# Kernel optimization log

Hardware: AMD Instinct MI355X
Metric: run time of the kernel (lower is better)

The kernel has to match this reference:

```python
import jax, jax.numpy as jnp
import numpy as np

BIG = 1e10  # penalty for cross-batch pairs in masked knn


def knn_interpolate(x, pos, pos_skip, batch, batch_skip, k):
    # squared pairwise distances [N_skip, N] via ||a||^2 + ||b||^2 - 2 a.b (avoids [Ns,N,3] temp)
    d2 = (jnp.sum(pos_skip**2, -1)[:, None]
          + jnp.sum(pos**2, -1)[None, :]
          - 2.0 * (pos_skip @ pos.T))
    d2 = jnp.maximum(d2, 0.0)
    # mask out neighbors from a different cloud in the batch
    d2 = d2 + jnp.where(batch_skip[:, None] != batch[None, :], BIG, 0.0)
    neg_d2k, idx = jax.lax.top_k(-d2, k)          # k smallest distances
    d2k = -neg_d2k                                # [N_skip, k]
    w = 1.0 / jnp.clip(d2k, 1e-16)                # inverse squared-distance weights (PyG convention)
    xk = x[idx]                                   # gather neighbor features [N_skip, k, C]
    return jnp.sum(w[..., None] * xk, axis=1) / jnp.sum(w, axis=1, keepdims=True)


def setup_inputs() -> dict:
    key = jax.random.key(0)
    ks = jax.random.split(key, 8)
    B, N, Ns, C, Cs, H = 4, 4096, 16384, 256, 128, 512
    x = jax.random.normal(ks[0], (N, C), dtype=jnp.float32)
    pos = jax.random.normal(ks[1], (N, 3), dtype=jnp.float32)
    batch = jnp.repeat(jnp.arange(B, dtype=jnp.int64), N // B)
    x_skip = jax.random.normal(ks[2], (Ns, Cs), dtype=jnp.float32)
    pos_skip = jax.random.normal(ks[3], (Ns, 3), dtype=jnp.float32)
    batch_skip = jnp.repeat(jnp.arange(B, dtype=jnp.int64), Ns // B)
    fan_in1, fan_in2 = C + Cs, H
    W1 = jax.random.normal(ks[4], (fan_in1, H), dtype=jnp.float32) / np.sqrt(fan_in1)
    b1 = jnp.zeros((H,), dtype=jnp.float32)
    W2 = jax.random.normal(ks[5], (H, H), dtype=jnp.float32) / np.sqrt(fan_in2)
    b2 = jnp.zeros((H,), dtype=jnp.float32)
    return {"x": x, "pos": pos, "batch": batch, "x_skip": x_skip,
            "pos_skip": pos_skip, "batch_skip": batch_skip,
            "W1": W1, "b1": b1, "W2": W2, "b2": b2, "k": 3}


def reference(x, pos, batch, x_skip, pos_skip, batch_skip, W1, b1, W2, b2, k):
    xi = knn_interpolate(x, pos, pos_skip, batch, batch_skip, k)  # [Ns, C]
    h = jnp.concatenate([xi, x_skip], axis=1)                     # [Ns, C+Cs]
    h = jax.nn.relu(h @ W1 + b1)
    h = jax.nn.relu(h @ W2 + b2)
    return (h, pos_skip, batch_skip)
```

## Files before the change

kernel.cpp:

```cpp
#include <hip/hip_runtime.h>
#include <hip/hip_bf16.h>
#include <float.h>


#define KNN_K 3
#define NBATCH 4

typedef __attribute__((ext_vector_type(8))) __bf16 bf16x8;
typedef __attribute__((ext_vector_type(4))) __bf16 bf16x4;
typedef __attribute__((ext_vector_type(4))) float  f32x4;
typedef unsigned long long ull;

__device__ __forceinline__ void gload_lds16(const void* g, void* l) {
    __builtin_amdgcn_global_load_lds(
        (const __attribute__((address_space(1))) unsigned int*)g,
        (__attribute__((address_space(3))) unsigned int*)l, 16, 0, 0);
}

template<int K>
__device__ __forceinline__ void insK(ull (&key)[K], ull c) {
    if (c < key[K-1]) {
        key[K-1] = c;
#pragma unroll
        for (int p = K-1; p >= 1; --p) {
            if (key[p] < key[p-1]) {
                ull t = key[p-1]; key[p-1] = key[p]; key[p] = t;
            }
        }
    }
}

template<int SPAN, int C, int Cs>
__global__ __launch_bounds__(256) void knn_wprep_fast(
    const float* __restrict__ x, const float* __restrict__ pos,
    const int* __restrict__ batch, const float* __restrict__ x_skip,
    const float* __restrict__ pos_skip, const int* __restrict__ batch_skip,
    __bf16* __restrict__ h0, float* __restrict__ out_tail, int Ns,
    const float* __restrict__ W1, const float* __restrict__ W2,
    __bf16* __restrict__ W1t, __bf16* __restrict__ W2t,
    int K1, int H, int H2, int knnBlocks)
{
    __shared__ float4 pos4[SPAN];
    __shared__ ull    skey[256 * KNN_K];
    __shared__ int    sidx[16][KNN_K];
    __shared__ float  swt [16][KNN_K + 1];
    __shared__ float  Ws[32][33];

    const int t = threadIdx.x;

    if (blockIdx.x >= knnBlocks) {
        int b = blockIdx.x - knnBlocks;
        const float* W; __bf16* Wt; int kt, nt, K, Ncols;
        const int nt1 = H / 32, n1 = (K1 / 32) * nt1;
        if (b < n1) { W = W1; Wt = W1t; K = K1; Ncols = H;  kt = b / nt1; nt = b % nt1; }
        else { b -= n1; const int nt2 = H2 / 32;
               W = W2; Wt = W2t; K = H;  Ncols = H2; kt = b / nt2; nt = b % nt2; }
        const int r = t >> 5, c = t & 31;
#pragma unroll
        for (int i = 0; i < 4; ++i)
            Ws[r + i*8][c] = W[(size_t)(kt*32 + r + i*8) * Ncols + nt*32 + c];
        __syncthreads();
#pragma unroll
        for (int i = 0; i < 4; ++i)
            Wt[(size_t)(nt*32 + r + i*8) * K + kt*32 + c] = (__bf16)Ws[c][r + i*8];
        return;
    }

    const int q0 = blockIdx.x * 16;
    const int bs    = batch_skip[q0];
    const int cbase = bs * SPAN;

    for (int i = t; i < SPAN; i += 256) {
        const int j = cbase + i;
        const float qx = pos[j*3+0], qy = pos[j*3+1], qz = pos[j*3+2];
        float pn2 = qx*qx + qy*qy + qz*qz;
        if (batch[j] != bs) pn2 = 3.0e38f;
        pos4[i] = make_float4(qx, qy, qz, pn2);
    }

    if (t < 48)               out_tail[q0*3 + t] = pos_skip[q0*3 + t];
    else if (t < 64)          out_tail[(size_t)Ns*3 + q0 + (t-48)] =
                                  (float)batch_skip[q0 + (t-48)];
    __syncthreads();

    const int q   = t & 15;
    const int g   = t >> 4;
    const int qq  = q0 + q;
    const float px = pos_skip[qq*3+0], py = pos_skip[qq*3+1], pz = pos_skip[qq*3+2];
    const float ps2 = px*px + py*py + pz*pz;

    ull kA[KNN_K], kB[KNN_K], kC[KNN_K], kD[KNN_K];
#pragma unroll
    for (int j = 0; j < KNN_K; ++j) { kA[j]=~0ull; kB[j]=~0ull; kC[j]=~0ull; kD[j]=~0ull; }

    const int base = g * (SPAN / 16);
#pragma unroll 4
    for (int i = 0; i < 16; ++i) {
        const int ii = (i + g) & 15;
        const int jA = base + ii;
        const int jB = base + 16 + ii;
        const int jC = base + 32 + ii;
        const int jD = base + 48 + ii;
        const float4 pA = pos4[jA];
        const float4 pB = pos4[jB];
        const float4 pC = pos4[jC];
        const float4 pD = pos4[jD];
        float d2A = (ps2 + pA.w) - 2.0f*(px*pA.x + py*pA.y + pz*pA.z);
        float d2B = (ps2 + pB.w) - 2.0f*(px*pB.x + py*pB.y + pz*pB.z);
        float d2C = (ps2 + pC.w) - 2.0f*(px*pC.x + py*pC.y + pz*pC.z);
        float d2D = (ps2 + pD.w) - 2.0f*(px*pD.x + py*pD.y + pz*pD.z);
        d2A = fmaxf(d2A, 0.0f); d2B = fmaxf(d2B, 0.0f);
        d2C = fmaxf(d2C, 0.0f); d2D = fmaxf(d2D, 0.0f);
        insK<KNN_K>(kA, ((ull)__float_as_uint(d2A) << 32) | (unsigned)(cbase + jA));
        insK<KNN_K>(kB, ((ull)__float_as_uint(d2B) << 32) | (unsigned)(cbase + jB));
        insK<KNN_K>(kC, ((ull)__float_as_uint(d2C) << 32) | (unsigned)(cbase + jC));
        insK<KNN_K>(kD, ((ull)__float_as_uint(d2D) << 32) | (unsigned)(cbase + jD));
    }
#pragma unroll
    for (int j = 0; j < KNN_K; ++j) insK<KNN_K>(kA, kB[j]);
#pragma unroll
    for (int j = 0; j < KNN_K; ++j) insK<KNN_K>(kA, kC[j]);
#pragma unroll
    for (int j = 0; j < KNN_K; ++j) insK<KNN_K>(kA, kD[j]);

#pragma unroll
    for (int j = 0; j < KNN_K; ++j) skey[t*KNN_K + j] = kA[j];
    __syncthreads();

    if (t < 16) {
        ull key[KNN_K];
#pragma unroll
        for (int j = 0; j < KNN_K; ++j) key[j] = skey[t*KNN_K + j];
#pragma unroll
        for (int gg = 1; gg < 16; ++gg)
#pragma unroll
            for (int j = 0; j < KNN_K; ++j)
                insK<KNN_K>(key, skey[(t + 16*gg)*KNN_K + j]);
        float wv[KNN_K]; float wsum = 0.0f;
#pragma unroll
        for (int j = 0; j < KNN_K; ++j) {
            const float d2 = __uint_as_float((unsigned)(key[j] >> 32));
            sidx[t][j] = (int)(key[j] & 0xFFFFFFFFull);
            wv[j] = 1.0f / fmaxf(d2, 1e-16f);
            wsum += wv[j];
            swt[t][j] = wv[j];
        }
        swt[t][KNN_K] = 1.0f / wsum;
    }
    __syncthreads();

    {
        const int gq  = t >> 4;
        const int sub = t & 15;
        const int s   = q0 + gq;
        const int i0 = sidx[gq][0], i1 = sidx[gq][1], i2 = sidx[gq][2];
        const float w0 = swt[gq][0], w1 = swt[gq][1], w2 = swt[gq][2];
        const float inv = swt[gq][3];
        __bf16* hrow = h0 + (size_t)s * (C + Cs);
        const float* x0 = &x[(size_t)i0*C];
        const float* x1 = &x[(size_t)i1*C];
        const float* x2 = &x[(size_t)i2*C];

#pragma unroll
        for (int cc = 0; cc < C; cc += 64) {
            const int c = cc + sub*4;
            const float4 v0 = *(const float4*)&x0[c];
            const float4 v1 = *(const float4*)&x1[c];
            const float4 v2 = *(const float4*)&x2[c];
            bf16x4 o;
            o[0] = (__bf16)((w0*v0.x + w1*v1.x + w2*v2.x) * inv);
            o[1] = (__bf16)((w0*v0.y + w1*v1.y + w2*v2.y) * inv);
            o[2] = (__bf16)((w0*v0.z + w1*v1.z + w2*v2.z) * inv);
            o[3] = (__bf16)((w0*v0.w + w1*v1.w + w2*v2.w) * inv);
            *(bf16x4*)&hrow[c] = o;
        }
#pragma unroll
        for (int cc = 0; cc < Cs; cc += 64) {
            const int c = cc + sub*4;
            const float4 v = *(const float4*)&x_skip[(size_t)s*Cs + c];
            bf16x4 o;
            o[0] = (__bf16)v.x; o[1] = (__bf16)v.y;
            o[2] = (__bf16)v.z; o[3] = (__bf16)v.w;
            *(bf16x4*)&hrow[C + c] = o;
        }
    }
}

__global__ __launch_bounds__(512) void knn_concat_kernel(
    const float* __restrict__ x, const float* __restrict__ pos,
    const int* __restrict__ batch, const float* __restrict__ x_skip,
    const float* __restrict__ pos_skip, const int* __restrict__ batch_skip,
    __bf16* __restrict__ h0, float* __restrict__ out_tail,
    int N, int C, int Cs, int Ns)
{
    const int t    = threadIdx.x;
    const int lane = t & 63;
    const int wav  = t >> 6;
    const int q0   = blockIdx.x * 64;
    const int q    = q0 + lane;

    __shared__ float4 pos4[1024];
    __shared__ ull    skey[512 * KNN_K];
    __shared__ int    sidx[64][KNN_K];
    __shared__ float  swt [64][KNN_K + 1];

    const int span  = N / NBATCH;
    const int bs    = batch_skip[q0];
    const int cbase = bs * span;

    for (int i = t; i < span; i += 512) {
        const int j = cbase + i;
        const float qx = pos[j*3+0], qy = pos[j*3+1], qz = pos[j*3+2];
        float pn2 = qx*qx + qy*qy + qz*qz;
        if (batch[j] != bs) pn2 = 3.0e38f;
        pos4[i] = make_float4(qx, qy, qz, pn2);
    }
    if (t < 192)              out_tail[q0*3 + t] = pos_skip[q0*3 + t];
    else if (t < 256)         out_tail[(size_t)Ns*3 + q0 + (t-192)] =
                                  (float)batch_skip[q0 + (t-192)];
    __syncthreads();

    const float px = pos_skip[q*3+0], py = pos_skip[q*3+1], pz = pos_skip[q*3+2];
    const float ps2 = px*px + py*py + pz*pz;

    ull key[KNN_K];
#pragma unroll
    for (int j = 0; j < KNN_K; ++j) key[j] = ~0ull;

    const int chunk = span / 8;
    const int c0    = wav * chunk;
#pragma unroll 4
    for (int i = 0; i < chunk; ++i) {
        const int jj = c0 + i;
        const float4 p = pos4[jj];
        const float dot = px*p.x + py*p.y + pz*p.z;
        float d2 = (ps2 + p.w) - 2.0f*dot;
        d2 = fmaxf(d2, 0.0f);
        insK<KNN_K>(key, ((ull)__float_as_uint(d2) << 32) | (unsigned)(cbase + jj));
    }
#pragma unroll
    for (int j = 0; j < KNN_K; ++j) skey[t*KNN_K + j] = key[j];
    __syncthreads();

    if (t < 64) {
#pragma unroll
        for (int ww = 1; ww < 8; ++ww)
#pragma unroll
            for (int j = 0; j < KNN_K; ++j)
                insK<KNN_K>(key, skey[(t + 64*ww)*KNN_K + j]);
        float wv[KNN_K]; float wsum = 0.0f;
#pragma unroll
        for (int j = 0; j < KNN_K; ++j) {
            const float d2 = __uint_as_float((unsigned)(key[j] >> 32));
            sidx[t][j] = (int)(key[j] & 0xFFFFFFFFull);
            wv[j] = 1.0f / fmaxf(d2, 1e-16f);
            wsum += wv[j];
            swt[t][j] = wv[j];
        }
        swt[t][KNN_K] = 1.0f / wsum;
    }
    __syncthreads();

    {
        const int gq  = t >> 3;
        const int sub = t & 7;
        const int s   = q0 + gq;
        const int i0 = sidx[gq][0], i1 = sidx[gq][1], i2 = sidx[gq][2];
        const float w0 = swt[gq][0], w1 = swt[gq][1], w2 = swt[gq][2];
        const float inv = swt[gq][3];
        __bf16* hrow = h0 + (size_t)s * (C + Cs);

        for (int c = sub*4; c < C; c += 32) {
            const float4 v0 = *(const float4*)&x[(size_t)i0*C + c];
            const float4 v1 = *(const float4*)&x[(size_t)i1*C + c];
            const float4 v2 = *(const float4*)&x[(size_t)i2*C + c];
            bf16x4 o;
            o[0] = (__bf16)((w0*v0.x + w1*v1.x + w2*v2.x) * inv);
            o[1] = (__bf16)((w0*v0.y + w1*v1.y + w2*v2.y) * inv);
            o[2] = (__bf16)((w0*v0.z + w1*v1.z + w2*v2.z) * inv);
            o[3] = (__bf16)((w0*v0.w + w1*v1.w + w2*v2.w) * inv);
            *(bf16x4*)&hrow[c] = o;
        }
        for (int c = sub*4; c < Cs; c += 32) {
            const float4 v = *(const float4*)&x_skip[(size_t)s*Cs + c];
            bf16x4 o;
            o[0] = (__bf16)v.x; o[1] = (__bf16)v.y;
            o[2] = (__bf16)v.z; o[3] = (__bf16)v.w;
            *(bf16x4*)&hrow[C + c] = o;
        }
    }
}

__global__ __launch_bounds__(256) void wprep_kernel(
    const float* __restrict__ W1, const float* __restrict__ W2,
    __bf16* __restrict__ W1t, __bf16* __restrict__ W2t,
    int K1, int H, int H2)
{
    __shared__ float Ws[32][33];
    int b = blockIdx.x;
    const float* W; __bf16* Wt; int kt, nt, K, Ncols;
    const int nt1 = H / 32, n1 = (K1 / 32) * nt1;
    if (b < n1) { W = W1; Wt = W1t; K = K1; Ncols = H;  kt = b / nt1; nt = b % nt1; }
    else { b -= n1; const int nt2 = H2 / 32;
           W = W2; Wt = W2t; K = H;  Ncols = H2; kt = b / nt2; nt = b % nt2; }

    const int t = threadIdx.x;
    const int r = t >> 5, c = t & 31;
#pragma unroll
    for (int i = 0; i < 4; ++i)
        Ws[r + i*8][c] = W[(size_t)(kt*32 + r + i*8) * Ncols + nt*32 + c];
    __syncthreads();
#pragma unroll
    for (int i = 0; i < 4; ++i)
        Wt[(size_t)(nt*32 + r + i*8) * K + kt*32 + c] = (__bf16)Ws[c][r + i*8];
}

template<bool OUT_BF16>
__global__ __launch_bounds__(256) void gemm_mfma64(
    const __bf16* __restrict__ A,
    const __bf16* __restrict__ Bt,
    const float* __restrict__ bias,
    void* __restrict__ Cout,
    int M, int N, int K, int GX)
{
    const int BK = 64;
    __shared__ __bf16 As[ 64 * BK];
    __shared__ __bf16 Bs[128 * BK];

    const int nwg = gridDim.x;
    int swz = blockIdx.x;
    if ((nwg & 7) == 0) swz = (blockIdx.x & 7) * (nwg >> 3) + (blockIdx.x >> 3);
    const int bx = swz % GX, by = swz / GX;

    const int t    = threadIdx.x;
    const int wave = t >> 6, lane = t & 63;
    const int row0 = by * 64;
    const int col0 = bx * 128;
    const int wr   = (wave >> 1) * 32;
    const int wc   = (wave & 1)  * 64;

    const int lr = lane & 15;
    const int lk = (lane >> 4) * 8;

    f32x4 acc[2][4] = {};

    for (int k0 = 0; k0 < K; k0 += BK) {
#pragma unroll
        for (int i = 0; i < 2; ++i) {
            const int ebase = (i*4 + wave) * 512;
            const int e  = ebase + lane*8;
            const int le = e ^ (((e >> 6) & 7) << 3);
            const int r  = le >> 6, c = le & 63;
            gload_lds16(&A[(size_t)(row0 + r)*K + k0 + c], &As[ebase]);
        }
#pragma unroll
        for (int i = 0; i < 4; ++i) {
            const int ebase = (i*4 + wave) * 512;
            const int e  = ebase + lane*8;
            const int le = e ^ (((e >> 6) & 7) << 3);
            const int r  = le >> 6, c = le & 63;
            gload_lds16(&Bt[(size_t)(col0 + r)*K + k0 + c], &Bs[ebase]);
        }
        __syncthreads();

#pragma unroll
        for (int kk = 0; kk < BK; kk += 32) {
            bf16x8 a[2], b[4];
#pragma unroll
            for (int m = 0; m < 2; ++m) {
                const int row = wr + m*16 + lr;
                const int col = (kk + lk) ^ ((row & 7) << 3);
                a[m] = *(const bf16x8*)&As[row*BK + col];
            }
#pragma unroll
            for (int n = 0; n < 4; ++n) {
                const int row = wc + n*16 + lr;
                const int col = (kk + lk) ^ ((row & 7) << 3);
                b[n] = *(const bf16x8*)&Bs[row*BK + col];
            }
#pragma unroll
            for (int m = 0; m < 2; ++m)
#pragma unroll
                for (int n = 0; n < 4; ++n)
                    acc[m][n] = __builtin_amdgcn_mfma_f32_16x16x32_bf16(
                        a[m], b[n], acc[m][n], 0, 0, 0);
        }
        __syncthreads();
    }

    const int orow = (lane >> 4) * 4;
#pragma unroll
    for (int m = 0; m < 2; ++m) {
#pragma unroll
        for (int n = 0; n < 4; ++n) {
            const int ccol = col0 + wc + n*16 + lr;
            const float bv = bias[ccol];
#pragma unroll
            for (int j = 0; j < 4; ++j) {
                const int crow = row0 + wr + m*16 + orow + j;
                const float v = fmaxf(acc[m][n][j] + bv, 0.0f);
                if (OUT_BF16) ((__bf16*)Cout)[(size_t)crow*N + ccol] = (__bf16)v;
                else          ((float*)Cout)[(size_t)crow*N + ccol]  = v;
            }
        }
    }
}

template<bool OUT_BF16>
__global__ __launch_bounds__(256) void gemm_mfma(
    const __bf16* __restrict__ A, const __bf16* __restrict__ Bt,
    const float* __restrict__ bias, void* __restrict__ Cout,
    int M, int N, int K)
{
    const int BK = 64;
    __shared__ __bf16 As[128 * BK];
    __shared__ __bf16 Bs[128 * BK];

    const int t    = threadIdx.x;
    const int wave = t >> 6, lane = t & 63;
    const int row0 = blockIdx.y * 128;
    const int col0 = blockIdx.x * 128;
    const int wr   = (wave >> 1) * 64;
    const int wc   = (wave & 1)  * 64;
    const int lr = lane & 15;
    const int lk = (lane >> 4) * 8;

    f32x4 acc[4][4] = {};

    for (int k0 = 0; k0 < K; k0 += BK) {
#pragma unroll
        for (int i = 0; i < 4; ++i) {
            const int ebase = (i*4 + wave) * 512;
            const int e  = ebase + lane*8;
            const int le = e ^ (((e >> 6) & 7) << 3);
            const int r  = le >> 6, c = le & 63;
            gload_lds16(&A[(size_t)(row0 + r)*K + k0 + c], &As[ebase]);
        }
#pragma unroll
        for (int i = 0; i < 4; ++i) {
            const int ebase = (i*4 + wave) * 512;
            const int e  = ebase + lane*8;
            const int le = e ^ (((e >> 6) & 7) << 3);
            const int r  = le >> 6, c = le & 63;
            gload_lds16(&Bt[(size_t)(col0 + r)*K + k0 + c], &Bs[ebase]);
        }
        __syncthreads();

#pragma unroll
        for (int kk = 0; kk < BK; kk += 32) {
            bf16x8 a[4], b[4];
#pragma unroll
            for (int m = 0; m < 4; ++m) {
                const int row = wr + m*16 + lr;
                const int col = (kk + lk) ^ ((row & 7) << 3);
                a[m] = *(const bf16x8*)&As[row*BK + col];
            }
#pragma unroll
            for (int n = 0; n < 4; ++n) {
                const int row = wc + n*16 + lr;
                const int col = (kk + lk) ^ ((row & 7) << 3);
                b[n] = *(const bf16x8*)&Bs[row*BK + col];
            }
#pragma unroll
            for (int m = 0; m < 4; ++m)
#pragma unroll
                for (int n = 0; n < 4; ++n)
                    acc[m][n] = __builtin_amdgcn_mfma_f32_16x16x32_bf16(
                        a[m], b[n], acc[m][n], 0, 0, 0);
        }
        __syncthreads();
    }

    const int orow = (lane >> 4) * 4;
#pragma unroll
    for (int m = 0; m < 4; ++m) {
#pragma unroll
        for (int n = 0; n < 4; ++n) {
            const int ccol = col0 + wc + n*16 + lr;
            const float bv = bias[ccol];
#pragma unroll
            for (int j = 0; j < 4; ++j) {
                const int crow = row0 + wr + m*16 + orow + j;
                const float v = fmaxf(acc[m][n][j] + bv, 0.0f);
                if (OUT_BF16) ((__bf16*)Cout)[(size_t)crow*N + ccol] = (__bf16)v;
                else          ((float*)Cout)[(size_t)crow*N + ccol]  = v;
            }
        }
    }
}

extern "C" void kernel_launch(void* const* d_in, const int* in_sizes, int n_in,
                              void* d_out, int out_size, void* d_ws, size_t ws_size,
                              hipStream_t stream)
{
    const float* x          = (const float*)d_in[0];
    const float* pos        = (const float*)d_in[1];
    const int*   batch      = (const int*)  d_in[2];
    const float* x_skip     = (const float*)d_in[3];
    const float* pos_skip   = (const float*)d_in[4];
    const int*   batch_skip = (const int*)  d_in[5];
    const float* W1         = (const float*)d_in[6];
    const float* b1         = (const float*)d_in[7];
    const float* W2         = (const float*)d_in[8];
    const float* b2         = (const float*)d_in[9];

    const int N  = in_sizes[2];
    const int Ns = in_sizes[5];
    const int C  = in_sizes[0] / N;
    const int Cs = in_sizes[3] / Ns;
    const int H  = in_sizes[7];
    const int H2 = in_sizes[9];
    const int K1 = C + Cs;

    __bf16* h0  = (__bf16*)d_ws;
    __bf16* h1  = h0  + (size_t)Ns * K1;
    __bf16* W1t = h1  + (size_t)Ns * H;
    __bf16* W2t = W1t + (size_t)H  * K1;
    float*  out = (float*)d_out;

    const int nblk_w = (K1 / 32) * (H / 32) + (H / 32) * (H2 / 32);

    if (N == 4096 && C == 256 && Cs == 128) {
        const int knnBlocks = Ns / 16;
        knn_wprep_fast<1024, 256, 128><<<knnBlocks + nblk_w, 256, 0, stream>>>(
            x, pos, batch, x_skip, pos_skip, batch_skip, h0,
            out + (size_t)Ns * H2, Ns,
            W1, W2, W1t, W2t, K1, H, H2, knnBlocks);
    } else {
        knn_concat_kernel<<<Ns / 64, 512, 0, stream>>>(
            x, pos, batch, x_skip, pos_skip, batch_skip, h0,
            out + (size_t)Ns * H2, N, C, Cs, Ns);
        wprep_kernel<<<nblk_w, 256, 0, stream>>>(W1, W2, W1t, W2t, K1, H, H2);
    }

    const bool gfast = ((Ns % 64) == 0 && (H % 128) == 0 && (H2 % 128) == 0 &&
                        (K1 % 64) == 0 && (H % 64) == 0);
    if (gfast) {
        const int g1 = (Ns / 64) * (H / 128);
        gemm_mfma64<true ><<<g1, 256, 0, stream>>>(h0, W1t, b1, (void*)h1,
                                                   Ns, H,  K1, H / 128);
        const int g2 = (Ns / 64) * (H2 / 128);
        gemm_mfma64<false><<<g2, 256, 0, stream>>>(h1, W2t, b2, (void*)out,
                                                   Ns, H2, H, H2 / 128);
    } else {
        dim3 g1(H  / 128, Ns / 128);
        gemm_mfma<true ><<<g1, 256, 0, stream>>>(h0, W1t, b1, (void*)h1, Ns, H,  K1);
        dim3 g2(H2 / 128, Ns / 128);
        gemm_mfma<false><<<g2, 256, 0, stream>>>(h1, W2t, b2, (void*)out, Ns, H2, H);
    }
}
```

Baseline: 50.66 us.

## Double-buffer LDS tiles in MFMA GEMM to overlap loads with compute

Doubles the shared-memory A and B tiles so the global-to-LDS loads for the next K step are issued before computing on the current step. Explicit vmcnt waits and raw barriers replace __syncthreads, so the next tile's loads stay in flight during the MFMA work. This aims to hide global memory latency in the two MLP GEMMs. In exchange, LDS use doubles, which may reduce occupancy, and the hand-placed waitcnt counts must match the number of issued loads.

```diff
diff --git a/kernel.cpp b/kernel.cpp
--- a/kernel.cpp
+++ b/kernel.cpp
@@ -324,8 +324,8 @@
     int M, int N, int K, int GX)
 {
     const int BK = 64;
-    __shared__ __bf16 As[ 64 * BK];
-    __shared__ __bf16 Bs[128 * BK];
+    __shared__ __bf16 As[2][ 64 * BK];
+    __shared__ __bf16 Bs[2][128 * BK];
 
     const int nwg = gridDim.x;
     int swz = blockIdx.x;
@@ -344,24 +344,38 @@
 
     f32x4 acc[2][4] = {};
 
-    for (int k0 = 0; k0 < K; k0 += BK) {
-#pragma unroll
-        for (int i = 0; i < 2; ++i) {
-            const int ebase = (i*4 + wave) * 512;
-            const int e  = ebase + lane*8;
-            const int le = e ^ (((e >> 6) & 7) << 3);
-            const int r  = le >> 6, c = le & 63;
-            gload_lds16(&A[(size_t)(row0 + r)*K + k0 + c], &As[ebase]);
-        }
-#pragma unroll
-        for (int i = 0; i < 4; ++i) {
-            const int ebase = (i*4 + wave) * 512;
-            const int e  = ebase + lane*8;
-            const int le = e ^ (((e >> 6) & 7) << 3);
-            const int r  = le >> 6, c = le & 63;
-            gload_lds16(&Bt[(size_t)(col0 + r)*K + k0 + c], &Bs[ebase]);
-        }
-        __syncthreads();
+    #define STAGE64(buf, k0)                                                   \
+    {                                                                          \
+        _Pragma("unroll")                                                      \
+        for (int i = 0; i < 2; ++i) {                                          \
+            const int ebase = (i*4 + wave) * 512;                              \
+            const int e  = ebase + lane*8;                                     \
+            const int le = e ^ (((e >> 6) & 7) << 3);                          \
+            const int r  = le >> 6, c = le & 63;                               \
+            gload_lds16(&A[(size_t)(row0 + r)*K + (k0) + c], &As[buf][ebase]); \
+        }                                                                      \
+        _Pragma("unroll")                                                      \
+        for (int i = 0; i < 4; ++i) {                                          \
+            const int ebase = (i*4 + wave) * 512;                              \
+            const int e  = ebase + lane*8;                                     \
+            const int le = e ^ (((e >> 6) & 7) << 3);                          \
+            const int r  = le >> 6, c = le & 63;                               \
+            gload_lds16(&Bt[(size_t)(col0 + r)*K + (k0) + c], &Bs[buf][ebase]);\
+        }                                                                      \
+    }
+
+    const int nsteps = K / BK;
+    STAGE64(0, 0);
+
+    for (int step = 0; step < nsteps; ++step) {
+        const int cur = step & 1;
+        if (step + 1 < nsteps) {
+            STAGE64(cur ^ 1, (step + 1) * BK);
+            asm volatile("s_waitcnt vmcnt(6)" ::: "memory");
+        } else {
+            asm volatile("s_waitcnt vmcnt(0)" ::: "memory");
+        }
+        __builtin_amdgcn_s_barrier();
 
 #pragma unroll
         for (int kk = 0; kk < BK; kk += 32) {
@@ -370,13 +384,13 @@
             for (int m = 0; m < 2; ++m) {
                 const int row = wr + m*16 + lr;
                 const int col = (kk + lk) ^ ((row & 7) << 3);
-                a[m] = *(const bf16x8*)&As[row*BK + col];
+                a[m] = *(const bf16x8*)&As[cur][row*BK + col];
             }
 #pragma unroll
             for (int n = 0; n < 4; ++n) {
                 const int row = wc + n*16 + lr;
                 const int col = (kk + lk) ^ ((row & 7) << 3);
-                b[n] = *(const bf16x8*)&Bs[row*BK + col];
+                b[n] = *(const bf16x8*)&Bs[cur][row*BK + col];
             }
 #pragma unroll
             for (int m = 0; m < 2; ++m)
@@ -385,8 +399,9 @@
                     acc[m][n] = __builtin_amdgcn_mfma_f32_16x16x32_bf16(
                         a[m], b[n], acc[m][n], 0, 0, 0);
         }
-        __syncthreads();
-    }
+        __builtin_amdgcn_s_barrier();
+    }
+    #undef STAGE64
 
     const int orow = (lane >> 4) * 4;
 #pragma unroll
```

After: 55.14 us. 1.09x slower.

## Halve queries per KNN block with two-level top-k merge and LDS aliasing

Applied to the files above, without the earlier changes.

Each KNN block now handles 8 query points instead of 16, so each thread scans 32 candidates in two chains instead of 64 in four. This doubles the KNN block count and shortens per-thread serial work. The final merge is split into two levels (64 threads merge 4 partials each, then 8 threads merge 8) instead of 16 threads merging 16 serially. The weight-transpose scratch aliases the pos4 LDS buffer to cut shared memory. The cost is more blocks, each reloading the 1024-point batch positions into LDS, plus extra barriers.

```diff
diff --git a/kernel.cpp b/kernel.cpp
--- a/kernel.cpp
+++ b/kernel.cpp
@@ -42,13 +42,13 @@
 {
     __shared__ float4 pos4[SPAN];
     __shared__ ull    skey[256 * KNN_K];
-    __shared__ int    sidx[16][KNN_K];
-    __shared__ float  swt [16][KNN_K + 1];
-    __shared__ float  Ws[32][33];
+    __shared__ int    sidx[8][KNN_K];
+    __shared__ float  swt [8][KNN_K + 1];
 
     const int t = threadIdx.x;
 
     if (blockIdx.x >= knnBlocks) {
+        float* Ws = (float*)pos4;
         int b = blockIdx.x - knnBlocks;
         const float* W; __bf16* Wt; int kt, nt, K, Ncols;
         const int nt1 = H / 32, n1 = (K1 / 32) * nt1;
@@ -58,15 +58,15 @@
         const int r = t >> 5, c = t & 31;
 #pragma unroll
         for (int i = 0; i < 4; ++i)
-            Ws[r + i*8][c] = W[(size_t)(kt*32 + r + i*8) * Ncols + nt*32 + c];
+            Ws[(r + i*8)*33 + c] = W[(size_t)(kt*32 + r + i*8) * Ncols + nt*32 + c];
         __syncthreads();
 #pragma unroll
         for (int i = 0; i < 4; ++i)
-            Wt[(size_t)(nt*32 + r + i*8) * K + kt*32 + c] = (__bf16)Ws[c][r + i*8];
+            Wt[(size_t)(nt*32 + r + i*8) * K + kt*32 + c] = (__bf16)Ws[c*33 + r + i*8];
         return;
     }
 
-    const int q0 = blockIdx.x * 16;
+    const int q0 = blockIdx.x * 8;
     const int bs    = batch_skip[q0];
     const int cbase = bs * SPAN;
 
@@ -78,64 +78,74 @@
         pos4[i] = make_float4(qx, qy, qz, pn2);
     }
 
-    if (t < 48)               out_tail[q0*3 + t] = pos_skip[q0*3 + t];
-    else if (t < 64)          out_tail[(size_t)Ns*3 + q0 + (t-48)] =
-                                  (float)batch_skip[q0 + (t-48)];
-    __syncthreads();
-
-    const int q   = t & 15;
-    const int g   = t >> 4;
-    const int qq  = q0 + q;
+    if (t < 24)               out_tail[q0*3 + t] = pos_skip[q0*3 + t];
+    else if (t < 32)          out_tail[(size_t)Ns*3 + q0 + (t-24)] =
+                                  (float)batch_skip[q0 + (t-24)];
+    __syncthreads();
+
+    const int q  = t & 7;
+    const int g  = t >> 3;
+    const int qq = q0 + q;
     const float px = pos_skip[qq*3+0], py = pos_skip[qq*3+1], pz = pos_skip[qq*3+2];
     const float ps2 = px*px + py*py + pz*pz;
 
-    ull kA[KNN_K], kB[KNN_K], kC[KNN_K], kD[KNN_K];
-#pragma unroll
-    for (int j = 0; j < KNN_K; ++j) { kA[j]=~0ull; kB[j]=~0ull; kC[j]=~0ull; kD[j]=~0ull; }
-
-    const int base = g * (SPAN / 16);
+    ull kA[KNN_K], kB[KNN_K];
+#pragma unroll
+    for (int j = 0; j < KNN_K; ++j) { kA[j] = ~0ull; kB[j] = ~0ull; }
+
+    const int base = g * 32;
 #pragma unroll 4
     for (int i = 0; i < 16; ++i) {
         const int ii = (i + g) & 15;
         const int jA = base + ii;
         const int jB = base + 16 + ii;
-        const int jC = base + 32 + ii;
-        const int jD = base + 48 + ii;
         const float4 pA = pos4[jA];
         const float4 pB = pos4[jB];
-        const float4 pC = pos4[jC];
-        const float4 pD = pos4[jD];
         float d2A = (ps2 + pA.w) - 2.0f*(px*pA.x + py*pA.y + pz*pA.z);
         float d2B = (ps2 + pB.w) - 2.0f*(px*pB.x + py*pB.y + pz*pB.z);
-        float d2C = (ps2 + pC.w) - 2.0f*(px*pC.x + py*pC.y + pz*pC.z);
-        float d2D = (ps2 + pD.w) - 2.0f*(px*pD.x + py*pD.y + pz*pD.z);
-        d2A = fmaxf(d2A, 0.0f); d2B = fmaxf(d2B, 0.0f);
-        d2C = fmaxf(d2C, 0.0f); d2D = fmaxf(d2D, 0.0f);
+        d2A = fmaxf(d2A, 0.0f);
+        d2B = fmaxf(d2B, 0.0f);
         insK<KNN_K>(kA, ((ull)__float_as_uint(d2A) << 32) | (unsigned)(cbase + jA));
         insK<KNN_K>(kB, ((ull)__float_as_uint(d2B) << 32) | (unsigned)(cbase + jB));
-        insK<KNN_K>(kC, ((ull)__float_as_uint(d2C) << 32) | (unsigned)(cbase + jC));
-        insK<KNN_K>(kD, ((ull)__float_as_uint(d2D) << 32) | (unsigned)(cbase + jD));
     }
 #pragma unroll
     for (int j = 0; j < KNN_K; ++j) insK<KNN_K>(kA, kB[j]);
-#pragma unroll
-    for (int j = 0; j < KNN_K; ++j) insK<KNN_K>(kA, kC[j]);
-#pragma unroll
-    for (int j = 0; j < KNN_K; ++j) insK<KNN_K>(kA, kD[j]);
 
 #pragma unroll
     for (int j = 0; j < KNN_K; ++j) skey[t*KNN_K + j] = kA[j];
     __syncthreads();
 
-    if (t < 16) {
+    ull m1[KNN_K];
+    if (t < 64) {
+        const int mq = t & 7, sg = t >> 3;
+#pragma unroll
+        for (int j = 0; j < KNN_K; ++j) m1[j] = ~0ull;
+#pragma unroll
+        for (int gg = 0; gg < 4; ++gg) {
+            const int slot = (sg*4 + gg)*8 + mq;
+#pragma unroll
+            for (int j = 0; j < KNN_K; ++j)
+                insK<KNN_K>(m1, skey[slot*KNN_K + j]);
+        }
+    }
+    __syncthreads();
+    if (t < 64) {
+#pragma unroll
+        for (int j = 0; j < KNN_K; ++j) skey[t*KNN_K + j] = m1[j];
+    }
+    __syncthreads();
+
+    if (t < 8) {
         ull key[KNN_K];
 #pragma unroll
-        for (int j = 0; j < KNN_K; ++j) key[j] = skey[t*KNN_K + j];
-#pragma unroll
-        for (int gg = 1; gg < 16; ++gg)
+        for (int j = 0; j < KNN_K; ++j) key[j] = ~0ull;
+#pragma unroll
+        for (int sg = 0; sg < 8; ++sg) {
+            const int slot = sg*8 + t;
 #pragma unroll
             for (int j = 0; j < KNN_K; ++j)
-                insK<KNN_K>(key, skey[(t + 16*gg)*KNN_K + j]);
+                insK<KNN_K>(key, skey[slot*KNN_K + j]);
+        }
         float wv[KNN_K]; float wsum = 0.0f;
 #pragma unroll
         for (int j = 0; j < KNN_K; ++j) {
@@ -150,8 +160,8 @@
     __syncthreads();
 
     {
-        const int gq  = t >> 4;
-        const int sub = t & 15;
+        const int gq  = t >> 5;
+        const int sub = t & 31;
         const int s   = q0 + gq;
         const int i0 = sidx[gq][0], i1 = sidx[gq][1], i2 = sidx[gq][2];
         const float w0 = swt[gq][0], w1 = swt[gq][1], w2 = swt[gq][2];
@@ -162,7 +172,7 @@
         const float* x2 = &x[(size_t)i2*C];
 
 #pragma unroll
-        for (int cc = 0; cc < C; cc += 64) {
+        for (int cc = 0; cc < C; cc += 128) {
             const int c = cc + sub*4;
             const float4 v0 = *(const float4*)&x0[c];
             const float4 v1 = *(const float4*)&x1[c];
@@ -175,7 +185,7 @@
             *(bf16x4*)&hrow[c] = o;
         }
 #pragma unroll
-        for (int cc = 0; cc < Cs; cc += 64) {
+        for (int cc = 0; cc < Cs; cc += 128) {
             const int c = cc + sub*4;
             const float4 v = *(const float4*)&x_skip[(size_t)s*Cs + c];
             bf16x4 o;
@@ -521,7 +531,7 @@
     const int nblk_w = (K1 / 32) * (H / 32) + (H / 32) * (H2 / 32);
 
     if (N == 4096 && C == 256 && Cs == 128) {
-        const int knnBlocks = Ns / 16;
+        const int knnBlocks = Ns / 8;
         knn_wprep_fast<1024, 256, 128><<<knnBlocks + nblk_w, 256, 0, stream>>>(
             x, pos, batch, x_skip, pos_skip, batch_skip, h0,
             out + (size_t)Ns * H2, Ns,
@@ -534,7 +544,7 @@
     }
 
     const bool gfast = ((Ns % 64) == 0 && (H % 128) == 0 && (H2 % 128) == 0 &&
-                        (K1 % 64) == 0 && (H % 64) == 0);
+                        (K1 % 64) == 0);
     if (gfast) {
         const int g1 = (Ns / 64) * (H / 128);
         gemm_mfma64<true ><<<g1, 256, 0, stream>>>(h0, W1t, b1, (void*)h1,
```

New measurement: 53.87 us. 6.3% more time.
